# Optimization experiments

Measured on AMD Instinct MI355X. Metric: run time of the kernel, lower is better.

The kernel has to match this reference:

```python
import jax, jax.numpy as jnp
import numpy as np

D_MODEL = 1024
N_HEAD = 16
D_HEAD = 64  # scale uses d_head even though heads are never split in this module
HD = N_HEAD * D_HEAD  # 1024
LN_EPS = 1e-5


def setup_inputs() -> dict:
    key = jax.random.key(0)
    ks = jax.random.split(key, 12)
    B, S = 8, 2048
    s = 0.02
    return {
        "q": jax.random.normal(ks[0], (B, S, D_MODEL), jnp.float32),
        "k": jax.random.normal(ks[1], (B, S, D_MODEL), jnp.float32),
        "v": jax.random.normal(ks[2], (B, S, D_MODEL), jnp.float32),
        "Wq": jax.random.normal(ks[3], (HD, D_MODEL), jnp.float32) * s,
        "Wk": jax.random.normal(ks[4], (HD, D_MODEL), jnp.float32) * s,
        "bk": jax.random.normal(ks[5], (HD,), jnp.float32) * s,
        "Wv": jax.random.normal(ks[6], (HD, D_MODEL), jnp.float32) * s,
        "bv": jax.random.normal(ks[7], (HD,), jnp.float32) * s,
        "Wo": jax.random.normal(ks[8], (D_MODEL, HD), jnp.float32) * s,
        "bo": jax.random.normal(ks[9], (D_MODEL,), jnp.float32) * s,
        "gamma": jnp.ones((D_MODEL,), jnp.float32),
        "beta": jnp.zeros((D_MODEL,), jnp.float32),
    }


def reference(q, k, v, Wq, Wk, bk, Wv, bv, Wo, bo, gamma, beta):
    scale = 1.0 / np.sqrt(D_HEAD).astype(np.float32)
    # projections (q_head has no bias, matching nn.Linear(bias=False))
    qh = jnp.einsum('bsm,hm->bsh', q, Wq) * scale      # [B,S,HD]
    kh = jnp.einsum('bsm,hm->bsh', k, Wk) + bk         # [B,S,HD]
    vh = jnp.einsum('bsm,hm->bsh', v, Wv) + bv         # [B,S,HD]
    # single effective head: full HD contraction (heads never split in source)
    scores = jnp.einsum('bid,bjd->bij', qh, kh)        # [B,Sq,Sk]
    dtype = scores.dtype
    probs = jax.nn.softmax(scores.astype(jnp.float32), axis=-1).astype(dtype)
    attn = jnp.einsum('bij,bjd->bid', probs, vh)       # [B,Sq,HD]
    attn_out = jnp.einsum('bsh,mh->bsm', attn, Wo) + bo
    x = q + attn_out                                   # dropout/drop_path = identity at eval
    mu = jnp.mean(x, axis=-1, keepdims=True)
    var = jnp.mean(jnp.square(x - mu), axis=-1, keepdims=True)
    return (x - mu) * jax.lax.rsqrt(var + LN_EPS) * gamma + beta
```

## Files before the change

### kernel.cpp

```cpp
#include <hip/hip_runtime.h>

typedef unsigned short u16;
typedef __attribute__((ext_vector_type(8))) short bf16x8;
typedef __attribute__((ext_vector_type(4))) short bf16x4;
typedef __attribute__((ext_vector_type(4))) float f32x4;

#define DEVINL static __device__ __forceinline__

DEVINL u16 f2bf(float x) {
  unsigned u = __float_as_uint(x);
  unsigned r = (u + 0x7FFFu + ((u >> 16) & 1u)) >> 16;
  return (u16)r;
}
DEVINL float bf2f(u16 h) { return __uint_as_float(((unsigned)h) << 16); }

DEVINL void gload_lds16(const u16* g, u16* l) {
  __builtin_amdgcn_global_load_lds(
      (const __attribute__((address_space(1))) void*)g,
      (__attribute__((address_space(3))) void*)l, 16, 0, 0);
}

DEVINL int swzg(int r, int s) {
  return ((r >> 1) << 3) + ((((r & 1) << 2) | s) ^ ((r >> 1) & 7));
}
DEVINL void g2rk(int g, int& row, int& ks) {
  int p = g >> 3, w = (g & 7) ^ (p & 7);
  row = p * 2 + (w >> 2);
  ks = w & 3;
}

DEVINL void stage_half(const u16* gbase, int K, u16* ldst, int tid) {
#pragma unroll
  for (int i = 0; i < 2; i++) {
    int g = i * 512 + tid;
    int row, ks;
    g2rk(g, row, ks);
    gload_lds16(gbase + (size_t)row * K + ks * 8, ldst + g * 8);
  }
}

template <bool A_F32, bool HAS_BIAS, bool RESID, bool OUT_F32, bool TRANSV>
__global__ __launch_bounds__(512, 2) void gemm_bt(
    const void* __restrict__ Ap_, const u16* __restrict__ Bp,
    const float* __restrict__ bias, const float* __restrict__ resid,
    void* __restrict__ Cp, int N, int K, long long Az, long long Bz,
    long long Cz, float scale) {
  const int gx = gridDim.x, gy = gridDim.y;
  int lin = blockIdx.x + gx * (blockIdx.y + gy * blockIdx.z);
  const int nwg = gx * gy * gridDim.z;
  if ((nwg & 7) == 0) {
    const int chunk = nwg >> 3;
    lin = (lin & 7) * chunk + (lin >> 3);
  }
  const int bz = lin / (gx * gy);
  const int rem = lin - bz * gx * gy;
  const int m0 = (rem / gx) * 256, n0 = (rem % gx) * 256;

  const int tid = threadIdx.x, lane = tid & 63, wv = tid >> 6;
  const int wr = wv >> 2, wc = wv & 3, lr = lane & 15, lh = lane >> 4;

  __shared__ u16 lds[3 * 16384];

  const u16* A16 = nullptr;
  const float* A32 = nullptr;
  if constexpr (A_F32)
    A32 = (const float*)Ap_ + (size_t)bz * Az + (size_t)m0 * K;
  else
    A16 = (const u16*)Ap_ + (size_t)bz * Az + (size_t)m0 * K;
  const u16* B = Bp + (size_t)bz * Bz + (size_t)n0 * K;

  f32x4 acc[8][4] = {};
  const int nt = K >> 5;

  if constexpr (A_F32) {
#pragma unroll
    for (int t = 0; t < 2; t++) {
      u16* dstA = &lds[t * 16384];
#pragma unroll
      for (int i = 0; i < 2; i++) {
        int g = i * 512 + tid, row, ks;
        g2rk(g, row, ks);
        const float* src = A32 + (size_t)row * K + t * 32 + ks * 8;
        f32x4 a = *(const f32x4*)src;
        f32x4 b = *(const f32x4*)(src + 4);
        bf16x8 h;
#pragma unroll
        for (int u = 0; u < 4; u++) {
          h[u] = (short)f2bf(a[u]);
          h[4 + u] = (short)f2bf(b[u]);
        }
        *(bf16x8*)&dstA[g * 8] = h;
      }
      stage_half(B + t * 32, K, &lds[t * 16384 + 8192], tid);
    }
    asm volatile("s_waitcnt vmcnt(2) lgkmcnt(0)" ::: "memory");
  } else {
    stage_half(A16, K, &lds[0], tid);
    stage_half(B, K, &lds[8192], tid);
    stage_half(A16 + 32, K, &lds[16384], tid);
    stage_half(B + 32, K, &lds[16384 + 8192], tid);
    asm volatile("s_waitcnt vmcnt(4)" ::: "memory");
  }
  __builtin_amdgcn_s_barrier();

  int d = 0;
  for (int t = 0; t < nt; ++t) {
    const u16* la = &lds[d * 16384];
    const u16* lb = la + 8192;
    int dn = d + 2;
    if (dn >= 3) dn -= 3;
    const bool doPre = (t + 2) < nt;

    bf16x8 bfv[4], af[4];
#pragma unroll
    for (int n = 0; n < 4; n++) {
      int row = wc * 64 + n * 16 + lr;
      bfv[n] = *(const bf16x8*)&lb[swzg(row, lh) * 8];
    }
#pragma unroll
    for (int m = 0; m < 4; m++) {
      int row = wr * 128 + m * 16 + lr;
      af[m] = *(const bf16x8*)&la[swzg(row, lh) * 8];
    }
    f32x4 pre0, pre1;
    if constexpr (A_F32) {
      if (doPre) {
        int row, ks;
        g2rk(tid, row, ks);
        const float* src = A32 + (size_t)row * K + (t + 2) * 32 + ks * 8;
        pre0 = *(const f32x4*)src;
        pre1 = *(const f32x4*)(src + 4);
      }
    } else {
      if (doPre) stage_half(A16 + (size_t)(t + 2) * 32, K, &lds[dn * 16384], tid);
    }
    __builtin_amdgcn_s_setprio(1);
#pragma unroll
    for (int m = 0; m < 4; m++)
#pragma unroll
      for (int n = 0; n < 4; n++)
        acc[m][n] = __builtin_amdgcn_mfma_f32_16x16x32_bf16(af[m], bfv[n],
                                                            acc[m][n], 0, 0, 0);
    __builtin_amdgcn_s_setprio(0);

#pragma unroll
    for (int m = 0; m < 4; m++) {
      int row = wr * 128 + (m + 4) * 16 + lr;
      af[m] = *(const bf16x8*)&la[swzg(row, lh) * 8];
    }
    if (doPre) stage_half(B + (size_t)(t + 2) * 32, K, &lds[dn * 16384 + 8192], tid);
    if constexpr (A_F32) {
      if (doPre) {
        u16* dstA = &lds[dn * 16384];
        bf16x8 h0;
#pragma unroll
        for (int u = 0; u < 4; u++) {
          h0[u] = (short)f2bf(pre0[u]);
          h0[4 + u] = (short)f2bf(pre1[u]);
        }
        *(bf16x8*)&dstA[tid * 8] = h0;
        int g = 512 + tid, row, ks;
        g2rk(g, row, ks);
        const float* src = A32 + (size_t)row * K + (t + 2) * 32 + ks * 8;
        f32x4 a = *(const f32x4*)src;
        f32x4 b = *(const f32x4*)(src + 4);
        bf16x8 h1;
#pragma unroll
        for (int u = 0; u < 4; u++) {
          h1[u] = (short)f2bf(a[u]);
          h1[4 + u] = (short)f2bf(b[u]);
        }
        *(bf16x8*)&dstA[g * 8] = h1;
      }
    }
    __builtin_amdgcn_s_setprio(1);
#pragma unroll
    for (int m = 0; m < 4; m++)
#pragma unroll
      for (int n = 0; n < 4; n++)
        acc[m + 4][n] = __builtin_amdgcn_mfma_f32_16x16x32_bf16(
            af[m], bfv[n], acc[m + 4][n], 0, 0, 0);
    __builtin_amdgcn_s_setprio(0);

    if constexpr (A_F32) {
      if (doPre)
        asm volatile("s_waitcnt vmcnt(2) lgkmcnt(0)" ::: "memory");
      else if (t + 1 < nt)
        asm volatile("s_waitcnt vmcnt(0) lgkmcnt(0)" ::: "memory");
    } else {
      if (doPre)
        asm volatile("s_waitcnt vmcnt(4)" ::: "memory");
      else if (t + 1 < nt)
        asm volatile("s_waitcnt vmcnt(0)" ::: "memory");
    }
    if (t + 1 < nt) __builtin_amdgcn_s_barrier();
    if (++d == 3) d = 0;
  }

  if constexpr (TRANSV) {
    u16* Ch = (u16*)Cp;
#pragma unroll
    for (int m = 0; m < 8; m++) {
      int row0 = m0 + wr * 128 + m * 16 + lh * 4;
      int b = row0 >> 11, s = row0 & 2047;
#pragma unroll
      for (int n = 0; n < 4; n++) {
        int col = n0 + wc * 64 + n * 16 + lr;
        bf16x4 pack;
#pragma unroll
        for (int j = 0; j < 4; j++) {
          float val = acc[m][n][j] * scale;
          if constexpr (HAS_BIAS) val += bias[col];
          pack[j] = (short)f2bf(val);
        }
        *(bf16x4*)&Ch[((size_t)b << 21) + ((size_t)col << 11) + s] = pack;
      }
    }
  } else {
    float* Cf = nullptr;
    u16* Ch = nullptr;
    if constexpr (OUT_F32)
      Cf = (float*)Cp + (size_t)bz * Cz;
    else
      Ch = (u16*)Cp + (size_t)bz * Cz;
#pragma unroll
    for (int m = 0; m < 8; m++) {
#pragma unroll
      for (int j = 0; j < 4; j++) {
        int row = m0 + wr * 128 + m * 16 + lh * 4 + j;
#pragma unroll
        for (int n = 0; n < 4; n++) {
          int col = n0 + wc * 64 + n * 16 + lr;
          float val = acc[m][n][j] * scale;
          if constexpr (HAS_BIAS) val += bias[col];
          if constexpr (RESID) val += resid[(size_t)row * N + col];
          if constexpr (OUT_F32)
            Cf[(size_t)row * N + col] = val;
          else
            Ch[(size_t)row * N + col] = f2bf(val);
        }
      }
    }
  }
}

__global__ __launch_bounds__(256) void cvt8w(const float* __restrict__ w0,
                                             const float* __restrict__ w1,
                                             const float* __restrict__ w2,
                                             const float* __restrict__ w3,
                                             u16* __restrict__ out) {
  const int wsel = blockIdx.x >> 9;
  const float* in = wsel == 0 ? w0 : wsel == 1 ? w1 : wsel == 2 ? w2 : w3;
  const size_t i = ((size_t)(blockIdx.x & 511) * 256 + threadIdx.x) * 8;
  f32x4 a = *(const f32x4*)&in[i];
  f32x4 b = *(const f32x4*)&in[i + 4];
  bf16x8 h;
#pragma unroll
  for (int u = 0; u < 4; u++) {
    h[u] = (short)f2bf(a[u]);
    h[4 + u] = (short)f2bf(b[u]);
  }
  *(bf16x8*)&out[(size_t)wsel * 1048576 + i] = h;
}

__global__ __launch_bounds__(256) void softmax_rows(u16* __restrict__ p) {
  const size_t base = (size_t)blockIdx.x * 2048;
  const int tid = threadIdx.x, lane = tid & 63, wv = tid >> 6;
  bf16x8 v = *(const bf16x8*)&p[base + tid * 8];
  float f[8];
#pragma unroll
  for (int u = 0; u < 8; u++) f[u] = bf2f((u16)v[u]);
  float mx = f[0];
#pragma unroll
  for (int u = 1; u < 8; u++) mx = fmaxf(mx, f[u]);
#pragma unroll
  for (int o = 32; o; o >>= 1) mx = fmaxf(mx, __shfl_xor(mx, o, 64));
  __shared__ float rm[4], rs[4];
  if (lane == 0) rm[wv] = mx;
  __syncthreads();
  mx = fmaxf(fmaxf(rm[0], rm[1]), fmaxf(rm[2], rm[3]));
  float s = 0.f, e[8];
#pragma unroll
  for (int u = 0; u < 8; u++) {
    e[u] = __expf(f[u] - mx);
    s += e[u];
  }
#pragma unroll
  for (int o = 32; o; o >>= 1) s += __shfl_xor(s, o, 64);
  if (lane == 0) rs[wv] = s;
  __syncthreads();
  s = rs[0] + rs[1] + rs[2] + rs[3];
  float inv = 1.f / s;
  bf16x8 o8;
#pragma unroll
  for (int u = 0; u < 8; u++) o8[u] = (short)f2bf(e[u] * inv);
  *(bf16x8*)&p[base + tid * 8] = o8;
}

__global__ __launch_bounds__(256) void ln_rows(const float* __restrict__ x,
                                               const float* __restrict__ gamma,
                                               const float* __restrict__ beta,
                                               float* __restrict__ out) {
  const size_t base = (size_t)blockIdx.x * 1024;
  const int tid = threadIdx.x, lane = tid & 63, wv = tid >> 6;
  f32x4 v = *(const f32x4*)&x[base + tid * 4];
  float s = v[0] + v[1] + v[2] + v[3];
  float q = v[0] * v[0] + v[1] * v[1] + v[2] * v[2] + v[3] * v[3];
#pragma unroll
  for (int o = 32; o; o >>= 1) {
    s += __shfl_xor(s, o, 64);
    q += __shfl_xor(q, o, 64);
  }
  __shared__ float rs[4], rq[4];
  if (lane == 0) {
    rs[wv] = s;
    rq[wv] = q;
  }
  __syncthreads();
  s = rs[0] + rs[1] + rs[2] + rs[3];
  q = rq[0] + rq[1] + rq[2] + rq[3];
  float mean = s * (1.f / 1024.f);
  float var = q * (1.f / 1024.f) - mean * mean;
  float rstd = rsqrtf(var + 1e-5f);
  f32x4 g = *(const f32x4*)&gamma[tid * 4];
  f32x4 b = *(const f32x4*)&beta[tid * 4];
  f32x4 o;
#pragma unroll
  for (int u = 0; u < 4; u++) o[u] = (v[u] - mean) * rstd * g[u] + b[u];
  *(f32x4*)&out[base + tid * 4] = o;
}

extern "C" void kernel_launch(void* const* d_in, const int* in_sizes, int n_in,
                              void* d_out, int out_size, void* d_ws,
                              size_t ws_size, hipStream_t stream) {
  (void)in_sizes; (void)n_in; (void)out_size; (void)ws_size;
  const float* q = (const float*)d_in[0];
  const float* k = (const float*)d_in[1];
  const float* v = (const float*)d_in[2];
  const float* Wq = (const float*)d_in[3];
  const float* Wk = (const float*)d_in[4];
  const float* bk = (const float*)d_in[5];
  const float* Wv = (const float*)d_in[6];
  const float* bv = (const float*)d_in[7];
  const float* Wo = (const float*)d_in[8];
  const float* bo = (const float*)d_in[9];
  const float* gamma = (const float*)d_in[10];
  const float* beta = (const float*)d_in[11];
  float* out = (float*)d_out;

  char* ws = (char*)d_ws;
  const size_t SZ_QKV = (size_t)16384 * 1024 * 2;
  u16* qh = (u16*)(ws);
  u16* kh = (u16*)(ws + SZ_QKV);
  u16* vhT = (u16*)(ws + 3 * SZ_QKV);
  u16* probs = (u16*)(ws + 4 * SZ_QKV);
  float* xbuf = (float*)(ws + 4 * SZ_QKV);
  u16* attn = qh;
  u16* Wqb = (u16*)(ws + 4 * SZ_QKV + (size_t)67108864);
  u16* Wkb = Wqb + 1048576;
  u16* Wvb = Wkb + 1048576;
  u16* Wob = Wvb + 1048576;

  cvt8w<<<2048, 256, 0, stream>>>(Wq, Wk, Wv, Wo, Wqb);

  dim3 gp(4, 64, 1);
  gemm_bt<true, false, false, false, false><<<gp, 512, 0, stream>>>(
      q, Wqb, nullptr, nullptr, qh, 1024, 1024, 0, 0, 0, 0.125f);
  gemm_bt<true, true, false, false, false><<<gp, 512, 0, stream>>>(
      k, Wkb, bk, nullptr, kh, 1024, 1024, 0, 0, 0, 1.0f);
  gemm_bt<true, true, false, false, true><<<gp, 512, 0, stream>>>(
      v, Wvb, bv, nullptr, vhT, 1024, 1024, 0, 0, 0, 1.0f);

  gemm_bt<false, false, false, false, false><<<dim3(8, 8, 8), 512, 0, stream>>>(
      qh, kh, nullptr, nullptr, probs, 2048, 1024, 2097152LL, 2097152LL,
      4194304LL, 1.0f);

  softmax_rows<<<16384, 256, 0, stream>>>(probs);

  gemm_bt<false, false, false, false, false><<<dim3(4, 8, 8), 512, 0, stream>>>(
      probs, vhT, nullptr, nullptr, attn, 1024, 2048, 4194304LL, 2097152LL,
      2097152LL, 1.0f);

  gemm_bt<false, true, true, true, false><<<dim3(4, 64, 1), 512, 0, stream>>>(
      attn, Wob, bo, q, xbuf, 1024, 1024, 0, 0, 0, 1.0f);

  ln_rows<<<16384, 256, 0, stream>>>(xbuf, gamma, beta, out);
}
```

Before: 414.7 us.

## Fuse softmax into score and PV GEMM epilogues using atomic row sums

The standalone softmax kernel is removed. The QK^T GEMM epilogue now writes exp(score) as bf16 and atomically accumulates per-row sums into a float buffer, and the PV GEMM epilogue divides by those sums. This drops a full read and write pass over the 8x2048x2048 probability matrix. It skips max subtraction, so it relies on scores staying small enough not to overflow exp, and it adds atomic contention plus a zeroing kernel.

```diff
diff --git a/kernel.cpp b/kernel.cpp
--- a/kernel.cpp
+++ b/kernel.cpp
@@ -39,12 +39,13 @@
   }
 }
 
-template <bool A_F32, bool HAS_BIAS, bool RESID, bool OUT_F32, bool TRANSV>
+template <bool A_F32, bool HAS_BIAS, bool RESID, bool OUT_F32, bool TRANSV,
+          int SMODE>
 __global__ __launch_bounds__(512, 2) void gemm_bt(
     const void* __restrict__ Ap_, const u16* __restrict__ Bp,
     const float* __restrict__ bias, const float* __restrict__ resid,
-    void* __restrict__ Cp, int N, int K, long long Az, long long Bz,
-    long long Cz, float scale) {
+    float* __restrict__ rsum, void* __restrict__ Cp, int N, int K,
+    long long Az, long long Bz, long long Cz, float scale) {
   const int gx = gridDim.x, gy = gridDim.y;
   int lin = blockIdx.x + gx * (blockIdx.y + gy * blockIdx.z);
   const int nwg = gx * gy * gridDim.z;
@@ -216,6 +217,28 @@
         *(bf16x4*)&Ch[((size_t)b << 21) + ((size_t)col << 11) + s] = pack;
       }
     }
+  } else if constexpr (SMODE == 1) {
+    u16* Ch = (u16*)Cp + (size_t)bz * Cz;
+#pragma unroll
+    for (int m = 0; m < 8; m++) {
+#pragma unroll
+      for (int j = 0; j < 4; j++) {
+        int row = m0 + wr * 128 + m * 16 + lh * 4 + j;
+        float ls = 0.f;
+#pragma unroll
+        for (int n = 0; n < 4; n++) {
+          int col = n0 + wc * 64 + n * 16 + lr;
+          float e = __expf(acc[m][n][j] * scale);
+          ls += e;
+          Ch[(size_t)row * N + col] = f2bf(e);
+        }
+        ls += __shfl_xor(ls, 1, 64);
+        ls += __shfl_xor(ls, 2, 64);
+        ls += __shfl_xor(ls, 4, 64);
+        ls += __shfl_xor(ls, 8, 64);
+        if (lr == 0) atomicAdd(&rsum[((size_t)bz << 11) + row], ls);
+      }
+    }
   } else {
     float* Cf = nullptr;
     u16* Ch = nullptr;
@@ -228,10 +251,13 @@
 #pragma unroll
       for (int j = 0; j < 4; j++) {
         int row = m0 + wr * 128 + m * 16 + lh * 4 + j;
+        float inv = 1.f;
+        if constexpr (SMODE == 2) inv = 1.0f / rsum[((size_t)bz << 11) + row];
 #pragma unroll
         for (int n = 0; n < 4; n++) {
           int col = n0 + wc * 64 + n * 16 + lr;
           float val = acc[m][n][j] * scale;
+          if constexpr (SMODE == 2) val *= inv;
           if constexpr (HAS_BIAS) val += bias[col];
           if constexpr (RESID) val += resid[(size_t)row * N + col];
           if constexpr (OUT_F32)
@@ -263,38 +289,9 @@
   *(bf16x8*)&out[(size_t)wsel * 1048576 + i] = h;
 }
 
-__global__ __launch_bounds__(256) void softmax_rows(u16* __restrict__ p) {
-  const size_t base = (size_t)blockIdx.x * 2048;
-  const int tid = threadIdx.x, lane = tid & 63, wv = tid >> 6;
-  bf16x8 v = *(const bf16x8*)&p[base + tid * 8];
-  float f[8];
-#pragma unroll
-  for (int u = 0; u < 8; u++) f[u] = bf2f((u16)v[u]);
-  float mx = f[0];
-#pragma unroll
-  for (int u = 1; u < 8; u++) mx = fmaxf(mx, f[u]);
-#pragma unroll
-  for (int o = 32; o; o >>= 1) mx = fmaxf(mx, __shfl_xor(mx, o, 64));
-  __shared__ float rm[4], rs[4];
-  if (lane == 0) rm[wv] = mx;
-  __syncthreads();
-  mx = fmaxf(fmaxf(rm[0], rm[1]), fmaxf(rm[2], rm[3]));
-  float s = 0.f, e[8];
-#pragma unroll
-  for (int u = 0; u < 8; u++) {
-    e[u] = __expf(f[u] - mx);
-    s += e[u];
-  }
-#pragma unroll
-  for (int o = 32; o; o >>= 1) s += __shfl_xor(s, o, 64);
-  if (lane == 0) rs[wv] = s;
-  __syncthreads();
-  s = rs[0] + rs[1] + rs[2] + rs[3];
-  float inv = 1.f / s;
-  bf16x8 o8;
-#pragma unroll
-  for (int u = 0; u < 8; u++) o8[u] = (short)f2bf(e[u] * inv);
-  *(bf16x8*)&p[base + tid * 8] = o8;
+__global__ __launch_bounds__(256) void zero_f32(float* __restrict__ p, int n) {
+  int i = blockIdx.x * 256 + threadIdx.x;
+  if (i < n) p[i] = 0.f;
 }
 
 __global__ __launch_bounds__(256) void ln_rows(const float* __restrict__ x,
@@ -352,6 +349,7 @@
   const size_t SZ_QKV = (size_t)16384 * 1024 * 2;
   u16* qh = (u16*)(ws);
   u16* kh = (u16*)(ws + SZ_QKV);
+  float* rowsum = (float*)(ws + 2 * SZ_QKV);
   u16* vhT = (u16*)(ws + 3 * SZ_QKV);
   u16* probs = (u16*)(ws + 4 * SZ_QKV);
   float* xbuf = (float*)(ws + 4 * SZ_QKV);
@@ -364,25 +362,27 @@
   cvt8w<<<2048, 256, 0, stream>>>(Wq, Wk, Wv, Wo, Wqb);
 
   dim3 gp(4, 64, 1);
-  gemm_bt<true, false, false, false, false><<<gp, 512, 0, stream>>>(
-      q, Wqb, nullptr, nullptr, qh, 1024, 1024, 0, 0, 0, 0.125f);
-  gemm_bt<true, true, false, false, false><<<gp, 512, 0, stream>>>(
-      k, Wkb, bk, nullptr, kh, 1024, 1024, 0, 0, 0, 1.0f);
-  gemm_bt<true, true, false, false, true><<<gp, 512, 0, stream>>>(
-      v, Wvb, bv, nullptr, vhT, 1024, 1024, 0, 0, 0, 1.0f);
-
-  gemm_bt<false, false, false, false, false><<<dim3(8, 8, 8), 512, 0, stream>>>(
-      qh, kh, nullptr, nullptr, probs, 2048, 1024, 2097152LL, 2097152LL,
-      4194304LL, 1.0f);
-
-  softmax_rows<<<16384, 256, 0, stream>>>(probs);
-
-  gemm_bt<false, false, false, false, false><<<dim3(4, 8, 8), 512, 0, stream>>>(
-      probs, vhT, nullptr, nullptr, attn, 1024, 2048, 4194304LL, 2097152LL,
-      2097152LL, 1.0f);
-
-  gemm_bt<false, true, true, true, false><<<dim3(4, 64, 1), 512, 0, stream>>>(
-      attn, Wob, bo, q, xbuf, 1024, 1024, 0, 0, 0, 1.0f);
+  gemm_bt<true, false, false, false, false, 0><<<gp, 512, 0, stream>>>(
+      q, Wqb, nullptr, nullptr, nullptr, qh, 1024, 1024, 0, 0, 0, 0.125f);
+  gemm_bt<true, true, false, false, false, 0><<<gp, 512, 0, stream>>>(
+      k, Wkb, bk, nullptr, nullptr, kh, 1024, 1024, 0, 0, 0, 1.0f);
+  gemm_bt<true, true, false, false, true, 0><<<gp, 512, 0, stream>>>(
+      v, Wvb, bv, nullptr, nullptr, vhT, 1024, 1024, 0, 0, 0, 1.0f);
+
+  zero_f32<<<64, 256, 0, stream>>>(rowsum, 16384);
+  gemm_bt<false, false, false, false, false, 1><<<dim3(8, 8, 8), 512, 0,
+                                                  stream>>>(
+      qh, kh, nullptr, nullptr, rowsum, probs, 2048, 1024, 2097152LL,
+      2097152LL, 4194304LL, 1.0f);
+
+  gemm_bt<false, false, false, false, false, 2><<<dim3(4, 8, 8), 512, 0,
+                                                  stream>>>(
+      probs, vhT, nullptr, nullptr, rowsum, attn, 1024, 2048, 4194304LL,
+      2097152LL, 2097152LL, 1.0f);
+
+  gemm_bt<false, true, true, true, false, 0><<<dim3(4, 64, 1), 512, 0,
+                                               stream>>>(
+      attn, Wob, bo, q, nullptr, xbuf, 1024, 1024, 0, 0, 0, 1.0f);
 
   ln_rows<<<16384, 256, 0, stream>>>(xbuf, gamma, beta, out);
 }
```

After: 407.8 us. Within noise of the previous version (-1.6%).
